# Performance work log

Hardware: AMD Instinct MI355X
Metric: run time of the kernel (lower is better)

The kernel has to match this reference:

```python
import jax, jax.numpy as jnp
import numpy as np

KS = 3  # kernel_size


def setup_inputs() -> dict:
    key = jax.random.key(0)
    ks = jax.random.split(key, 3)
    B, C, H, W = 32, 256, 128, 128
    x = jax.random.normal(ks[0], (B, C, H, W), dtype=jnp.float32)
    w1 = jax.random.normal(ks[1], (C, C), dtype=jnp.float32) * (1.0 / np.sqrt(C))
    b1 = jnp.zeros((C,), dtype=jnp.float32)
    w2 = jax.random.normal(ks[2], (C, KS * KS), dtype=jnp.float32) * (1.0 / np.sqrt(C))
    b2 = jnp.zeros((KS * KS,), dtype=jnp.float32)
    return {"x": x, "w1": w1, "b1": b1, "w2": w2, "b2": b2}


def reference(x, w1, b1, w2, b2):
    B, C, H, W = x.shape
    # kernel generator: global avg pool -> 1x1 conv (C->C) -> relu -> 1x1 conv (C->k^2)
    pooled = x.mean(axis=(2, 3))                       # [B, C]
    z = jax.nn.relu(pooled @ w1 + b1)                  # [B, C]
    kernels = (z @ w2 + b2).reshape(B, 1, KS, KS)      # [B, 1, k, k] per-sample kernels
    # per-sample 3x3 conv on channel-mean map via grouped conv (groups = B)
    x_mean = x.mean(axis=1).reshape(1, B, H, W)        # [1, B, H, W]
    att = jax.lax.conv_general_dilated(
        x_mean, kernels,
        window_strides=(1, 1),
        padding=((KS // 2, KS // 2), (KS // 2, KS // 2)),
        feature_group_count=B,
        dimension_numbers=("NCHW", "OIHW", "NCHW"),
    )                                                   # [1, B, H, W]
    att = jax.nn.sigmoid(att.reshape(B, 1, H, W))
    return x * att
```

## Files before the change

kernel.cpp:

```cpp
#include <hip/hip_runtime.h>
#include <math.h>

#define B 32
#define C 256
#define H 128
#define W 128
#define HW (H * W)

#define WS_POOLED 0
#define WS_KER    8192
#define WS_XMEAN  16384

__global__ __launch_bounds__(256) void k1_reduce(const float* __restrict__ x,
                                                 float* __restrict__ pooled_sum,
                                                 float* __restrict__ x_mean) {
    const int blk   = blockIdx.x;
    const int b     = blk >> 4;
    const int chunk = blk & 15;
    const int hw0   = chunk * 1024;
    const int t     = threadIdx.x;
    const int lane  = t & 63;
    const int wave  = t >> 6;

    __shared__ float pooled_lds[4][C];

    const float* xb = x + (size_t)b * C * HW + hw0 + 4 * t;

    float m0 = 0.f, m1 = 0.f, m2 = 0.f, m3 = 0.f;
    #pragma unroll 4
    for (int c = 0; c < C; ++c) {
        const float4 v = *(const float4*)(xb + (size_t)c * HW);
        m0 += v.x; m1 += v.y; m2 += v.z; m3 += v.w;
        float s = (v.x + v.y) + (v.z + v.w);
        #pragma unroll
        for (int m = 32; m >= 1; m >>= 1)
            s += __shfl_xor(s, m, 64);
        if (lane == 0) pooled_lds[wave][c] = s;
    }

    const float invC = 1.0f / (float)C;
    float4 xm;
    xm.x = m0 * invC; xm.y = m1 * invC; xm.z = m2 * invC; xm.w = m3 * invC;
    *(float4*)(x_mean + (size_t)b * HW + hw0 + 4 * t) = xm;

    __syncthreads();
    const float p = pooled_lds[0][t] + pooled_lds[1][t] +
                    pooled_lds[2][t] + pooled_lds[3][t];
    atomicAdd(&pooled_sum[b * C + t], p);
}

__global__ __launch_bounds__(256) void k2_mlp(const float* __restrict__ pooled_sum,
                                              const float* __restrict__ w1,
                                              const float* __restrict__ b1,
                                              const float* __restrict__ w2,
                                              const float* __restrict__ b2,
                                              float* __restrict__ kernels) {
    const int b = blockIdx.x;
    const int t = threadIdx.x;
    __shared__ float p[C];
    __shared__ float z[C];

    p[t] = pooled_sum[b * C + t] * (1.0f / (float)HW);
    __syncthreads();

    float acc = b1[t];
    #pragma unroll 8
    for (int c = 0; c < C; ++c)
        acc = fmaf(p[c], w1[c * C + t], acc);
    z[t] = fmaxf(acc, 0.f);
    __syncthreads();

    if (t < 9) {
        float k = b2[t];
        for (int j = 0; j < C; ++j)
            k = fmaf(z[j], w2[j * 9 + t], k);
        kernels[b * 9 + t] = k;
    }
}

#define ROWS 8
#define CSPLIT 4
#define CPB (C / CSPLIT)

__global__ __launch_bounds__(256) void k3_apply(const float* __restrict__ x,
                                                const float* __restrict__ x_mean,
                                                const float* __restrict__ kernels,
                                                float* __restrict__ out) {
    const int blk  = blockIdx.x;
    const int cs   = blk & (CSPLIT - 1);
    const int rb   = (blk >> 2) & 15;
    const int b    = blk >> 6;
    const int row0 = rb * ROWS;
    const int t    = threadIdx.x;

    __shared__ __align__(16) float att[ROWS * W];
    __shared__ float ker[9];
    if (t < 9) ker[t] = kernels[b * 9 + t];
    __syncthreads();

    const float* xm = x_mean + (size_t)b * HW;
    #pragma unroll
    for (int i = 0; i < 4; ++i) {
        const int p = t + i * 256;
        const int h = row0 + (p >> 7);
        const int w = p & 127;
        float a = 0.f;
        #pragma unroll
        for (int dy = 0; dy < 3; ++dy) {
            const int hh = h + dy - 1;
            if (hh < 0 || hh >= H) continue;
            #pragma unroll
            for (int dx = 0; dx < 3; ++dx) {
                const int ww = w + dx - 1;
                if (ww < 0 || ww >= W) continue;
                a = fmaf(xm[hh * W + ww], ker[dy * 3 + dx], a);
            }
        }
        att[p] = 1.0f / (1.0f + __expf(-a));
    }
    __syncthreads();

    const float4 av = ((const float4*)att)[t];
    const size_t base = (size_t)b * C * HW + (size_t)row0 * W + 4 * t;
    const int c0 = cs * CPB;
    #pragma unroll 4
    for (int c = c0; c < c0 + CPB; ++c) {
        const float4 v = *(const float4*)(x + base + (size_t)c * HW);
        float4 o;
        o.x = v.x * av.x; o.y = v.y * av.y; o.z = v.z * av.z; o.w = v.w * av.w;
        *(float4*)(out + base + (size_t)c * HW) = o;
    }
}

extern "C" void kernel_launch(void* const* d_in, const int* in_sizes, int n_in,
                              void* d_out, int out_size, void* d_ws, size_t ws_size,
                              hipStream_t stream) {
    const float* x  = (const float*)d_in[0];
    const float* w1 = (const float*)d_in[1];
    const float* b1 = (const float*)d_in[2];
    const float* w2 = (const float*)d_in[3];
    const float* b2 = (const float*)d_in[4];
    float* out = (float*)d_out;
    float* ws  = (float*)d_ws;

    float* pooled = ws + WS_POOLED;
    float* kers   = ws + WS_KER;
    float* xmean  = ws + WS_XMEAN;

    hipMemsetAsync(pooled, 0, B * C * sizeof(float), stream);
    k1_reduce<<<B * 16, 256, 0, stream>>>(x, pooled, xmean);
    k2_mlp<<<B, 256, 0, stream>>>(pooled, w1, b1, w2, b2, kers);
    k3_apply<<<B * 16 * CSPLIT, 256, 0, stream>>>(x, xmean, kers, out);
}
```

Before: 1.113 ms.

## Split reduction by channel slices, precompute attention map, use nontemporal loads/stores

The reduction kernel now partitions each sample by channel slices instead of spatial chunks. Each block writes a partial channel-sum map to workspace and writes its pooled sums directly, which removes the atomics and the memset. A new kernel sums the partials, applies the 3x3 conv with an LDS halo tile and sigmoid, and stores the attention map once. The apply kernel then just loads that map, and the large x/out streams use nontemporal loads and stores. This adds a 32MB partial buffer write and read-back plus an extra launch, in exchange for simpler streaming and no redundant per-channel-split conv work.

```diff
diff --git a/kernel.cpp b/kernel.cpp
--- a/kernel.cpp
+++ b/kernel.cpp
@@ -7,46 +7,60 @@
 #define W 128
 #define HW (H * W)
 
+#define CSLICES 16
+#define CPS (C / CSLICES)
+
+typedef float f32x4 __attribute__((ext_vector_type(4)));
+
 #define WS_POOLED 0
 #define WS_KER    8192
-#define WS_XMEAN  16384
+#define WS_ATT    16384
+#define WS_PART   540672
 
 __global__ __launch_bounds__(256) void k1_reduce(const float* __restrict__ x,
                                                  float* __restrict__ pooled_sum,
-                                                 float* __restrict__ x_mean) {
-    const int blk   = blockIdx.x;
-    const int b     = blk >> 4;
-    const int chunk = blk & 15;
-    const int hw0   = chunk * 1024;
-    const int t     = threadIdx.x;
-    const int lane  = t & 63;
-    const int wave  = t >> 6;
+                                                 float* __restrict__ part) {
+    const int blk = blockIdx.x;
+    const int b   = blk >> 4;
+    const int cs  = blk & 15;
+    const int t   = threadIdx.x;
 
-    __shared__ float pooled_lds[4][C];
+    __shared__ float plds[CPS][257];
 
-    const float* xb = x + (size_t)b * C * HW + hw0 + 4 * t;
+    const float* xb = x + (size_t)b * C * HW + (size_t)cs * CPS * HW + 4 * t;
 
-    float m0 = 0.f, m1 = 0.f, m2 = 0.f, m3 = 0.f;
-    #pragma unroll 4
-    for (int c = 0; c < C; ++c) {
-        const float4 v = *(const float4*)(xb + (size_t)c * HW);
-        m0 += v.x; m1 += v.y; m2 += v.z; m3 += v.w;
-        float s = (v.x + v.y) + (v.z + v.w);
+    f32x4 xm[16];
+    #pragma unroll
+    for (int i = 0; i < 16; ++i) xm[i] = (f32x4)(0.f);
+
+    #pragma unroll 2
+    for (int ch = 0; ch < CPS; ++ch) {
+        const float* xc = xb + (size_t)ch * HW;
+        float p = 0.f;
         #pragma unroll
-        for (int m = 32; m >= 1; m >>= 1)
-            s += __shfl_xor(s, m, 64);
-        if (lane == 0) pooled_lds[wave][c] = s;
+        for (int i = 0; i < 16; ++i) {
+            const f32x4 v =
+                __builtin_nontemporal_load((const f32x4*)(xc + i * 1024));
+            xm[i] += v;
+            p += (v.x + v.y) + (v.z + v.w);
+        }
+        plds[ch][t] = p;
     }
 
-    const float invC = 1.0f / (float)C;
-    float4 xm;
-    xm.x = m0 * invC; xm.y = m1 * invC; xm.z = m2 * invC; xm.w = m3 * invC;
-    *(float4*)(x_mean + (size_t)b * HW + hw0 + 4 * t) = xm;
+    float* pp = part + ((size_t)cs * B + b) * HW + 4 * t;
+    #pragma unroll
+    for (int i = 0; i < 16; ++i)
+        *(f32x4*)(pp + i * 1024) = xm[i];
 
     __syncthreads();
-    const float p = pooled_lds[0][t] + pooled_lds[1][t] +
-                    pooled_lds[2][t] + pooled_lds[3][t];
-    atomicAdd(&pooled_sum[b * C + t], p);
+    const int ch = t >> 4;
+    const int g  = t & 15;
+    float s = 0.f;
+    #pragma unroll
+    for (int j = 0; j < 16; ++j) s += plds[ch][g + 16 * j];
+    #pragma unroll
+    for (int m = 8; m >= 1; m >>= 1) s += __shfl_xor(s, m, 64);
+    if (g == 0) pooled_sum[b * C + cs * CPS + ch] = s;
 }
 
 __global__ __launch_bounds__(256) void k2_mlp(const float* __restrict__ pooled_sum,
@@ -78,13 +92,59 @@
     }
 }
 
+__global__ __launch_bounds__(256) void k2b_att(const float* __restrict__ part,
+                                               const float* __restrict__ kernels,
+                                               float* __restrict__ att) {
+    const int blk  = blockIdx.x;
+    const int rb   = blk & 15;
+    const int b    = blk >> 4;
+    const int row0 = rb * 8;
+    const int t    = threadIdx.x;
+
+    __shared__ float xm_t[10][132];
+    __shared__ float ker[9];
+    if (t < 9) ker[t] = kernels[b * 9 + t];
+
+    for (int idx = t; idx < 10 * 132; idx += 256) ((float*)xm_t)[idx] = 0.f;
+    __syncthreads();
+
+    const float invC = 1.0f / (float)C;
+    for (int idx = t; idx < 1280; idx += 256) {
+        const int r  = idx >> 7;
+        const int wl = idx & 127;
+        const int hh = row0 - 1 + r;
+        if (hh >= 0 && hh < H) {
+            float s = 0.f;
+            #pragma unroll
+            for (int sl = 0; sl < CSLICES; ++sl)
+                s += part[((size_t)sl * B + b) * HW + hh * W + wl];
+            xm_t[r][1 + wl] = s * invC;
+        }
+    }
+    __syncthreads();
+
+    #pragma unroll
+    for (int i = 0; i < 4; ++i) {
+        const int pos = t + i * 256;
+        const int h   = pos >> 7;
+        const int w   = pos & 127;
+        float a = 0.f;
+        #pragma unroll
+        for (int dy = 0; dy < 3; ++dy)
+            #pragma unroll
+            for (int dx = 0; dx < 3; ++dx)
+                a = fmaf(xm_t[h + dy][w + dx], ker[dy * 3 + dx], a);
+        att[(size_t)b * HW + (size_t)(row0 + h) * W + w] =
+            1.0f / (1.0f + __expf(-a));
+    }
+}
+
 #define ROWS 8
 #define CSPLIT 4
 #define CPB (C / CSPLIT)
 
 __global__ __launch_bounds__(256) void k3_apply(const float* __restrict__ x,
-                                                const float* __restrict__ x_mean,
-                                                const float* __restrict__ kernels,
+                                                const float* __restrict__ att,
                                                 float* __restrict__ out) {
     const int blk  = blockIdx.x;
     const int cs   = blk & (CSPLIT - 1);
@@ -93,48 +153,23 @@
     const int row0 = rb * ROWS;
     const int t    = threadIdx.x;
 
-    __shared__ __align__(16) float att[ROWS * W];
-    __shared__ float ker[9];
-    if (t < 9) ker[t] = kernels[b * 9 + t];
-    __syncthreads();
-
-    const float* xm = x_mean + (size_t)b * HW;
-    #pragma unroll
-    for (int i = 0; i < 4; ++i) {
-        const int p = t + i * 256;
-        const int h = row0 + (p >> 7);
-        const int w = p & 127;
-        float a = 0.f;
-        #pragma unroll
-        for (int dy = 0; dy < 3; ++dy) {
-            const int hh = h + dy - 1;
-            if (hh < 0 || hh >= H) continue;
-            #pragma unroll
-            for (int dx = 0; dx < 3; ++dx) {
-                const int ww = w + dx - 1;
-                if (ww < 0 || ww >= W) continue;
-                a = fmaf(xm[hh * W + ww], ker[dy * 3 + dx], a);
-            }
-        }
-        att[p] = 1.0f / (1.0f + __expf(-a));
-    }
-    __syncthreads();
-
-    const float4 av = ((const float4*)att)[t];
+    const f32x4 av =
+        *(const f32x4*)(att + (size_t)b * HW + (size_t)row0 * W + 4 * t);
     const size_t base = (size_t)b * C * HW + (size_t)row0 * W + 4 * t;
     const int c0 = cs * CPB;
     #pragma unroll 4
     for (int c = c0; c < c0 + CPB; ++c) {
-        const float4 v = *(const float4*)(x + base + (size_t)c * HW);
-        float4 o;
-        o.x = v.x * av.x; o.y = v.y * av.y; o.z = v.z * av.z; o.w = v.w * av.w;
-        *(float4*)(out + base + (size_t)c * HW) = o;
+        const f32x4 v = __builtin_nontemporal_load(
+            (const f32x4*)(x + base + (size_t)c * HW));
+        const f32x4 o = v * av;
+        __builtin_nontemporal_store(o, (f32x4*)(out + base + (size_t)c * HW));
     }
 }
 
 extern "C" void kernel_launch(void* const* d_in, const int* in_sizes, int n_in,
                               void* d_out, int out_size, void* d_ws, size_t ws_size,
                               hipStream_t stream) {
+    (void)in_sizes; (void)n_in; (void)out_size; (void)ws_size;
     const float* x  = (const float*)d_in[0];
     const float* w1 = (const float*)d_in[1];
     const float* b1 = (const float*)d_in[2];
@@ -145,10 +180,11 @@
 
     float* pooled = ws + WS_POOLED;
     float* kers   = ws + WS_KER;
-    float* xmean  = ws + WS_XMEAN;
+    float* att    = ws + WS_ATT;
+    float* part   = ws + WS_PART;
 
-    hipMemsetAsync(pooled, 0, B * C * sizeof(float), stream);
-    k1_reduce<<<B * 16, 256, 0, stream>>>(x, pooled, xmean);
+    k1_reduce<<<B * CSLICES, 256, 0, stream>>>(x, pooled, part);
     k2_mlp<<<B, 256, 0, stream>>>(pooled, w1, b1, w2, b2, kers);
-    k3_apply<<<B * 16 * CSPLIT, 256, 0, stream>>>(x, xmean, kers, out);
+    k2b_att<<<B * 16, 256, 0, stream>>>(part, kers, att);
+    k3_apply<<<B * 16 * CSPLIT, 256, 0, stream>>>(x, att, out);
 }
```

Measured after the change: 1.025 ms. 7.9% less time.
